# Performance work log

Measured on AMD Instinct MI355X. Metric: run time of the kernel, lower is better.

## Reference

```python
import jax, jax.numpy as jnp
import numpy as np

V, D, U1, U2, GLU_U = 50257, 50, 32, 64, 128
B, T = 1024, 1024


def setup_inputs() -> dict:
    key = jax.random.key(0)
    ks = jax.random.split(key, 10)
    g = lambda k, shape, fan: (jax.random.normal(k, shape, jnp.float32) / np.sqrt(fan)).astype(jnp.float32)
    return dict(
        tokens=jax.random.randint(ks[0], (B, T), 0, V),
        emb=g(ks[1], (V, D), D),
        kx1=g(ks[2], (D, 3 * U1), D),
        kh1=g(ks[3], (U1, 3 * U1), U1),
        b1=jnp.zeros((2, 3 * U1), jnp.float32),
        kx2=g(ks[4], (U1, 3 * U2), U1),
        kh2=g(ks[5], (U2, 3 * U2), U2),
        b2=jnp.zeros((2, 3 * U2), jnp.float32),
        wg=g(ks[6], (U2, 2 * GLU_U), U2),
        bg=jnp.zeros((2 * GLU_U,), jnp.float32),
        wd=g(ks[7], (GLU_U, 1), GLU_U),
        bd=jnp.zeros((1,), jnp.float32),
    )


def _gru(x, kx, kh, b, return_sequences):
    # Keras GRU, reset_after=True (default): gates ordered [z, r, h].
    u = kh.shape[0]
    xproj = jnp.einsum('btd,dk->btk', x, kx) + b[0]  # [B,T,3u] input projections, precomputed
    bh = b[1]

    def step(h, xt):
        hm = h @ kh + bh                                   # [B,3u]
        z = jax.nn.sigmoid(xt[:, :u] + hm[:, :u])
        r = jax.nn.sigmoid(xt[:, u:2 * u] + hm[:, u:2 * u])
        hh = jnp.tanh(xt[:, 2 * u:] + r * hm[:, 2 * u:])   # reset applied after recurrent matmul
        hn = z * h + (1.0 - z) * hh
        return hn, hn

    h0 = jnp.zeros((x.shape[0], u), x.dtype)
    hT, ys = jax.lax.scan(step, h0, jnp.swapaxes(xproj, 0, 1))
    return jnp.swapaxes(ys, 0, 1) if return_sequences else hT


def reference(tokens, emb, kx1, kh1, b1, kx2, kh2, b2, wg, bg, wd, bd):
    x = emb[tokens]                         # [B,T,50]
    x = _gru(x, kx1, kh1, b1, True)         # [B,T,32]
    x = _gru(x, kx2, kh2, b2, False)        # [B,64] (last hidden state)
    a = x @ wg + bg                         # GLU: [B,256]
    x = a[:, :GLU_U] * jax.nn.sigmoid(a[:, GLU_U:])
    return jax.nn.sigmoid(x @ wd + bd)      # [B,1]
```

## Files before the change

### kernel.cpp

```cpp
#include <hip/hip_runtime.h>

#define VV 50257
#define DD 50
#define TT 1024
#define BB 1024

typedef float v4f __attribute__((ext_vector_type(4)));

__device__ __forceinline__ float rl(float v, int lane) {
    return __int_as_float(__builtin_amdgcn_readlane(__float_as_int(v), lane));
}
__device__ __forceinline__ float sigmf(float x) { return 1.0f / (1.0f + __expf(-x)); }
__device__ __forceinline__ float tanhf_fast(float x) {
    float e = __expf(-2.0f * fabsf(x));
    return copysignf((1.0f - e) / (1.0f + e), x);
}

__global__ void proj_emb(const float* __restrict__ emb, const float* __restrict__ kx1,
                         const float* __restrict__ b1, float* __restrict__ P1) {
    int j = threadIdx.x;
    int v0 = blockIdx.x * 8;
    #pragma unroll 1
    for (int vv = 0; vv < 8; ++vv) {
        int v = v0 + vv;
        if (v >= VV) return;
        float acc = b1[j];
        #pragma unroll
        for (int d = 0; d < DD; ++d)
            acc += emb[v * DD + d] * kx1[d * 96 + j];
        P1[v * 96 + j] = acc;
    }
}

__global__ __launch_bounds__(128, 1)
void rnn_main(const int* __restrict__ tokens, const float* __restrict__ P1,
              const float* __restrict__ kh1, const float* __restrict__ b1,
              const float* __restrict__ kx2, const float* __restrict__ kh2,
              const float* __restrict__ b2, const float* __restrict__ wg,
              const float* __restrict__ bg, const float* __restrict__ wd,
              const float* __restrict__ bd, float* __restrict__ out) {
    const int lane = threadIdx.x & 63;
    const int wv   = threadIdx.x >> 6;
    const int row  = blockIdx.x;
    const int l32  = lane & 31;
    const int* __restrict__ trow = tokens + row * TT;

    __shared__ float4 xb[4][64];
    __shared__ __align__(16) float h2s[64];
    __shared__ __align__(16) float h1s[32];

    float w[192];
    float f0, f1, f2, f3 = 0.f, f4 = 0.f;

    if (wv == 0) {
        h2s[lane] = 0.f;
        #pragma unroll
        for (int k = 0; k < 64; ++k) {
            w[3 * k]     = kh2[k * 192 + lane];
            w[3 * k + 1] = kh2[k * 192 + 64 + lane];
            w[3 * k + 2] = kh2[k * 192 + 128 + lane];
        }
        f0 = b2[192 + lane];
        f1 = b2[256 + lane];
        f2 = b2[320 + lane];
    } else {
        if (lane < 32) h1s[lane] = 0.f;
        #pragma unroll
        for (int k = 0; k < 32; ++k) {
            w[k]          = kh1[k * 96 + lane];
            w[32 + k]     = (lane < 32) ? kh1[k * 96 + 64 + lane] : 0.f;
            w[64 + 3 * k] = kx2[k * 192 + lane];
            w[65 + 3 * k] = kx2[k * 192 + 64 + lane];
            w[66 + 3 * k] = kx2[k * 192 + 128 + lane];
        }
        f0 = b1[96 + lane];
        f1 = (lane < 32) ? b1[160 + lane] : 0.f;
        f2 = b2[lane];
        f3 = b2[64 + lane];
        f4 = b2[128 + lane];
    }

    float h1 = 0.f, h2 = 0.f;
    float pz = 0.f, pr = 0.f, ph = 0.f;
    int tokc = 0;
    if (wv == 1) {
        const float* __restrict__ p = P1 + trow[0] * 96;
        pz = p[l32]; pr = p[32 + l32]; ph = p[64 + l32];
        tokc = trow[1];
    }

    float mz, mr, mh;

    #pragma unroll 1
    for (int t = -1; t < TT; ++t) {
        if (wv == 0) {
            if (t >= 0) {
                const v4f* __restrict__ h2v = reinterpret_cast<const v4f*>(h2s);
                mz = f0; mr = f1; mh = f2;
                #pragma unroll
                for (int kc = 0; kc < 16; ++kc) {
                    v4f hb = h2v[kc];
                    const int b = kc * 12;
                    mz += hb.x * w[b];     mr += hb.x * w[b + 1];  mh += hb.x * w[b + 2];
                    mz += hb.y * w[b + 3]; mr += hb.y * w[b + 4];  mh += hb.y * w[b + 5];
                    mz += hb.z * w[b + 6]; mr += hb.z * w[b + 7];  mh += hb.z * w[b + 8];
                    mz += hb.w * w[b + 9]; mr += hb.w * w[b + 10]; mh += hb.w * w[b + 11];
                }
            }
        } else if (t < TT) {
            const v4f* __restrict__ h1v = reinterpret_cast<const v4f*>(h1s);
            v4f hb[8];
            #pragma unroll
            for (int kc = 0; kc < 8; ++kc) hb[kc] = h1v[kc];
            if (t >= 0) {
                float xz = f2, xr = f3, xh = f4;
                #pragma unroll
                for (int kc = 0; kc < 8; ++kc) {
                    const int b = 64 + kc * 12;
                    xz += hb[kc].x * w[b];     xr += hb[kc].x * w[b + 1];  xh += hb[kc].x * w[b + 2];
                    xz += hb[kc].y * w[b + 3]; xr += hb[kc].y * w[b + 4];  xh += hb[kc].y * w[b + 5];
                    xz += hb[kc].z * w[b + 6]; xr += hb[kc].z * w[b + 7];  xh += hb[kc].z * w[b + 8];
                    xz += hb[kc].w * w[b + 9]; xr += hb[kc].w * w[b + 10]; xh += hb[kc].w * w[b + 11];
                }
                xb[t & 3][lane] = make_float4(xz, xr, xh, 0.f);
            }
            if (t < TT - 1) {
                float az = f0, ah = f1;
                #pragma unroll
                for (int kc = 0; kc < 8; ++kc) {
                    az += hb[kc].x * w[4 * kc];     ah += hb[kc].x * w[32 + 4 * kc];
                    az += hb[kc].y * w[4 * kc + 1]; ah += hb[kc].y * w[32 + 4 * kc + 1];
                    az += hb[kc].z * w[4 * kc + 2]; ah += hb[kc].z * w[32 + 4 * kc + 2];
                    az += hb[kc].w * w[4 * kc + 3]; ah += hb[kc].w * w[32 + 4 * kc + 3];
                }
                float ra  = __shfl_xor(az, 32);
                float z1  = sigmf(pz + az);
                float g1  = sigmf(pr + ra);
                float hh1 = tanhf_fast(ph + g1 * ah);
                h1 = z1 * h1 + (1.f - z1) * hh1;
                if (lane < 32) h1s[lane] = h1;
                const float* __restrict__ pn = P1 + tokc * 96;
                pz = pn[l32]; pr = pn[32 + l32]; ph = pn[64 + l32];
                tokc = trow[(t + 3 < TT) ? (t + 3) : (TT - 1)];
            }
        }
        __syncthreads();
        if (wv == 0 && t >= 0) {
            float4 x  = xb[t & 3][lane];
            float z2  = sigmf(x.x + mz);
            float r2  = sigmf(x.y + mr);
            float hh2 = tanhf_fast(x.z + r2 * mh);
            h2 = z2 * h2 + (1.f - z2) * hh2;
            h2s[lane] = h2;
        }
    }

    if (wv == 0) {
        float a0 = bg[lane], a1 = bg[64 + lane], a2 = bg[128 + lane], a3 = bg[192 + lane];
        #pragma unroll
        for (int k = 0; k < 64; ++k) {
            float s = rl(h2, k);
            a0 += s * wg[k * 256 + lane];
            a1 += s * wg[k * 256 + 64 + lane];
            a2 += s * wg[k * 256 + 128 + lane];
            a3 += s * wg[k * 256 + 192 + lane];
        }
        float g = a0 * sigmf(a2) * wd[lane] + a1 * sigmf(a3) * wd[64 + lane];
        g += __shfl_xor(g, 32); g += __shfl_xor(g, 16); g += __shfl_xor(g, 8);
        g += __shfl_xor(g, 4);  g += __shfl_xor(g, 2);  g += __shfl_xor(g, 1);
        if (lane == 0) out[row] = sigmf(g + bd[0]);
    }
}

extern "C" void kernel_launch(void* const* d_in, const int* in_sizes, int n_in,
                              void* d_out, int out_size, void* d_ws, size_t ws_size,
                              hipStream_t stream) {
    const int*   tokens = (const int*)d_in[0];
    const float* emb = (const float*)d_in[1];
    const float* kx1 = (const float*)d_in[2];
    const float* kh1 = (const float*)d_in[3];
    const float* b1  = (const float*)d_in[4];
    const float* kx2 = (const float*)d_in[5];
    const float* kh2 = (const float*)d_in[6];
    const float* b2  = (const float*)d_in[7];
    const float* wg  = (const float*)d_in[8];
    const float* bg  = (const float*)d_in[9];
    const float* wd  = (const float*)d_in[10];
    const float* bd  = (const float*)d_in[11];
    float* out = (float*)d_out;
    float* P1  = (float*)d_ws;

    proj_emb<<<(VV + 7) / 8, 96, 0, stream>>>(emb, kx1, b1, P1);
    rnn_main<<<BB, 128, 0, stream>>>(tokens, P1, kh1, b1, kx2, kh2, b2,
                                     wg, bg, wd, bd, out);
}
```

Measured before the change: 1.025 ms.

## Replace per-step block barrier with producer/consumer flags between GRU wavefronts

The two wavefronts (layer-1 GRU plus layer-2 input projection, and layer-2 recurrence) no longer meet at a __syncthreads every timestep. They communicate through an 8-deep LDS ring of projected inputs, using shared prod/cons counters with spin-waits, so the two layers can drift up to 8 steps apart and the lockstep barrier stall goes away. The risks are spin-wait overhead from s_sleep polling and memory-ordering subtleties in LDS. There is also a possible race: wave 0 writes h2s inside its own loop while reading it in the next iteration, which is fine within a single wave.

```diff
diff --git a/kernel.cpp b/kernel.cpp
--- a/kernel.cpp
+++ b/kernel.cpp
@@ -45,9 +45,13 @@
     const int l32  = lane & 31;
     const int* __restrict__ trow = tokens + row * TT;
 
-    __shared__ float4 xb[4][64];
+    __shared__ float4 xb[8][64];
     __shared__ __align__(16) float h2s[64];
     __shared__ __align__(16) float h1s[32];
+    __shared__ int prod;
+    __shared__ int cons;
+
+    if (threadIdx.x == 0) { prod = 0; cons = 0; }
 
     float w[192];
     float f0, f1, f2, f3 = 0.f, f4 = 0.f;
@@ -80,39 +84,28 @@
         f4 = b2[128 + lane];
     }
 
-    float h1 = 0.f, h2 = 0.f;
-    float pz = 0.f, pr = 0.f, ph = 0.f;
-    int tokc = 0;
+    __syncthreads();
+
     if (wv == 1) {
-        const float* __restrict__ p = P1 + trow[0] * 96;
-        pz = p[l32]; pr = p[32 + l32]; ph = p[64 + l32];
-        tokc = trow[1];
-    }
-
-    float mz, mr, mh;
-
-    #pragma unroll 1
-    for (int t = -1; t < TT; ++t) {
-        if (wv == 0) {
-            if (t >= 0) {
-                const v4f* __restrict__ h2v = reinterpret_cast<const v4f*>(h2s);
-                mz = f0; mr = f1; mh = f2;
-                #pragma unroll
-                for (int kc = 0; kc < 16; ++kc) {
-                    v4f hb = h2v[kc];
-                    const int b = kc * 12;
-                    mz += hb.x * w[b];     mr += hb.x * w[b + 1];  mh += hb.x * w[b + 2];
-                    mz += hb.y * w[b + 3]; mr += hb.y * w[b + 4];  mh += hb.y * w[b + 5];
-                    mz += hb.z * w[b + 6]; mr += hb.z * w[b + 7];  mh += hb.z * w[b + 8];
-                    mz += hb.w * w[b + 9]; mr += hb.w * w[b + 10]; mh += hb.w * w[b + 11];
-                }
-            }
-        } else if (t < TT) {
+        float h1 = 0.f;
+        float pz, pr, ph;
+        {
+            const float* __restrict__ p = P1 + trow[0] * 96;
+            pz = p[l32]; pr = p[32 + l32]; ph = p[64 + l32];
+        }
+        int tokc = trow[1];
+
+        #pragma unroll 1
+        for (int t = -1; t < TT; ++t) {
             const v4f* __restrict__ h1v = reinterpret_cast<const v4f*>(h1s);
             v4f hb[8];
             #pragma unroll
             for (int kc = 0; kc < 8; ++kc) hb[kc] = h1v[kc];
             if (t >= 0) {
+                if (t >= 8) {
+                    int need = t - 7;
+                    while (*(volatile int*)&cons < need) { __builtin_amdgcn_s_sleep(1); }
+                }
                 float xz = f2, xr = f3, xh = f4;
                 #pragma unroll
                 for (int kc = 0; kc < 8; ++kc) {
@@ -122,7 +115,9 @@
                     xz += hb[kc].z * w[b + 6]; xr += hb[kc].z * w[b + 7];  xh += hb[kc].z * w[b + 8];
                     xz += hb[kc].w * w[b + 9]; xr += hb[kc].w * w[b + 10]; xh += hb[kc].w * w[b + 11];
                 }
-                xb[t & 3][lane] = make_float4(xz, xr, xh, 0.f);
+                xb[t & 7][lane] = make_float4(xz, xr, xh, 0.f);
+                __threadfence_block();
+                if (lane == 0) *(volatile int*)&prod = t + 1;
             }
             if (t < TT - 1) {
                 float az = f0, ah = f1;
@@ -144,32 +139,47 @@
                 tokc = trow[(t + 3 < TT) ? (t + 3) : (TT - 1)];
             }
         }
-        __syncthreads();
-        if (wv == 0 && t >= 0) {
-            float4 x  = xb[t & 3][lane];
-            float z2  = sigmf(x.x + mz);
-            float r2  = sigmf(x.y + mr);
-            float hh2 = tanhf_fast(x.z + r2 * mh);
-            h2 = z2 * h2 + (1.f - z2) * hh2;
-            h2s[lane] = h2;
-        }
-    }
-
-    if (wv == 0) {
-        float a0 = bg[lane], a1 = bg[64 + lane], a2 = bg[128 + lane], a3 = bg[192 + lane];
-        #pragma unroll
-        for (int k = 0; k < 64; ++k) {
-            float s = rl(h2, k);
-            a0 += s * wg[k * 256 + lane];
-            a1 += s * wg[k * 256 + 64 + lane];
-            a2 += s * wg[k * 256 + 128 + lane];
-            a3 += s * wg[k * 256 + 192 + lane];
-        }
-        float g = a0 * sigmf(a2) * wd[lane] + a1 * sigmf(a3) * wd[64 + lane];
-        g += __shfl_xor(g, 32); g += __shfl_xor(g, 16); g += __shfl_xor(g, 8);
-        g += __shfl_xor(g, 4);  g += __shfl_xor(g, 2);  g += __shfl_xor(g, 1);
-        if (lane == 0) out[row] = sigmf(g + bd[0]);
-    }
+        return;
+    }
+
+    float h2 = 0.f;
+    #pragma unroll 1
+    for (int t = 0; t < TT; ++t) {
+        const v4f* __restrict__ h2v = reinterpret_cast<const v4f*>(h2s);
+        float mz = f0, mr = f1, mh = f2;
+        #pragma unroll
+        for (int kc = 0; kc < 16; ++kc) {
+            v4f hb = h2v[kc];
+            const int b = kc * 12;
+            mz += hb.x * w[b];     mr += hb.x * w[b + 1];  mh += hb.x * w[b + 2];
+            mz += hb.y * w[b + 3]; mr += hb.y * w[b + 4];  mh += hb.y * w[b + 5];
+            mz += hb.z * w[b + 6]; mr += hb.z * w[b + 7];  mh += hb.z * w[b + 8];
+            mz += hb.w * w[b + 9]; mr += hb.w * w[b + 10]; mh += hb.w * w[b + 11];
+        }
+        while (*(volatile int*)&prod < t + 1) { __builtin_amdgcn_s_sleep(1); }
+        __threadfence_block();
+        float4 x  = xb[t & 7][lane];
+        float z2  = sigmf(x.x + mz);
+        float r2  = sigmf(x.y + mr);
+        float hh2 = tanhf_fast(x.z + r2 * mh);
+        h2 = z2 * h2 + (1.f - z2) * hh2;
+        h2s[lane] = h2;
+        if (lane == 0) *(volatile int*)&cons = t + 1;
+    }
+
+    float a0 = bg[lane], a1 = bg[64 + lane], a2 = bg[128 + lane], a3 = bg[192 + lane];
+    #pragma unroll
+    for (int k = 0; k < 64; ++k) {
+        float s = rl(h2, k);
+        a0 += s * wg[k * 256 + lane];
+        a1 += s * wg[k * 256 + 64 + lane];
+        a2 += s * wg[k * 256 + 128 + lane];
+        a3 += s * wg[k * 256 + 192 + lane];
+    }
+    float g = a0 * sigmf(a2) * wd[lane] + a1 * sigmf(a3) * wd[64 + lane];
+    g += __shfl_xor(g, 32); g += __shfl_xor(g, 16); g += __shfl_xor(g, 8);
+    g += __shfl_xor(g, 4);  g += __shfl_xor(g, 2);  g += __shfl_xor(g, 1);
+    if (lane == 0) out[row] = sigmf(g + bd[0]);
 }
 
 extern "C" void kernel_launch(void* const* d_in, const int* in_sizes, int n_in,
```

After: 1.722 ms. +68.0%, slower.
